# Kernel optimization log

Hardware: AMD Instinct MI355X
Metric: run time of the kernel (lower is better)

The kernel has to match this reference:

```python
import jax, jax.numpy as jnp
import numpy as np

N_NODES = 50000
N_EDGES = 600000
D_IN = 128
D_HID = 128
D_OUT = 64


def setup_inputs() -> dict:
    key = jax.random.key(0)
    ks = jax.random.split(key, 8)
    x = jax.random.normal(ks[0], (N_NODES, D_IN), dtype=jnp.float32)
    edge_index = jax.random.randint(ks[1], (2, N_EDGES), 0, N_NODES, dtype=jnp.int32)
    s = 0.05
    W1l = jax.random.normal(ks[2], (D_HID, D_IN), dtype=jnp.float32) * s
    b1 = jnp.zeros((D_HID,), dtype=jnp.float32)
    W1r = jax.random.normal(ks[3], (D_HID, D_IN), dtype=jnp.float32) * s
    W2l = jax.random.normal(ks[4], (D_OUT, D_HID), dtype=jnp.float32) * s
    b2 = jnp.zeros((D_OUT,), dtype=jnp.float32)
    W2r = jax.random.normal(ks[5], (D_OUT, D_HID), dtype=jnp.float32) * s
    return {"x": x, "edge_index": edge_index, "W1l": W1l, "b1": b1,
            "W1r": W1r, "W2l": W2l, "b2": b2, "W2r": W2r}


def _sage_conv(x, src, dst, Wl, bl, Wr, n_nodes):
    # mean aggregation of source features at destination nodes
    msg_sum = jax.ops.segment_sum(x[src], dst, num_segments=n_nodes)  # [N, D]
    deg = jax.ops.segment_sum(jnp.ones((src.shape[0], 1), x.dtype), dst,
                              num_segments=n_nodes)                   # [N, 1]
    mean = msg_sum / jnp.maximum(deg, 1.0)
    # out = lin_l(mean_neighbors) + lin_r(x_self); bias only on lin_l (PyG default)
    return mean @ Wl.T + bl + x @ Wr.T


def reference(x, edge_index, W1l, b1, W1r, W2l, b2, W2r):
    src, dst = edge_index[0], edge_index[1]
    n = x.shape[0]
    h = jax.nn.relu(_sage_conv(x, src, dst, W1l, b1, W1r, n))
    # dropout p=0.5 is identity in eval mode (training=False)
    return _sage_conv(h, src, dst, W2l, b2, W2r, n)
```

## Files before the change

kernel.cpp:

```cpp
#include <hip/hip_runtime.h>
#include <hip/hip_bf16.h>

typedef __bf16 bf16x8 __attribute__((ext_vector_type(8)));
typedef float f32x4 __attribute__((ext_vector_type(4)));

#define D_FEAT 128
#define MT_STRIDE 136
#define CHUNK 1024

__device__ __forceinline__ float bf16_to_f(unsigned int u16) {
    union { unsigned int i; float f; } c; c.i = u16 << 16; return c.f;
}
__device__ __forceinline__ unsigned short f_to_bf16(float f) {
    __hip_bfloat16 h = (__hip_bfloat16)f;
    return *(unsigned short*)&h;
}
__device__ __forceinline__ float ld(const void* p, int is16, size_t i) {
    return is16 ? (float)((const __hip_bfloat16*)p)[i] : ((const float*)p)[i];
}

__global__ void probe_kernel(const void* x, int* flags) {
    if (threadIdx.x < 64) {
        const unsigned short* u = (const unsigned short*)x;
        unsigned short v = u[threadIdx.x * 2];
        int e = (v >> 7) & 0xFF;
        bool plaus = (e >= 100 && e <= 140);
        unsigned long long m = __ballot(plaus);
        if (threadIdx.x == 0) {
            flags[0] = (__popcll(m) >= 48) ? 1 : 0;
            flags[1] = 1;
        }
    }
}

__global__ void prep_kernel(const void* W1l, const void* b1, const void* W1r,
                            const void* W2l, const void* b2, const void* W2r,
                            const int* __restrict__ flags, unsigned short* wout) {
    int i = blockIdx.x * blockDim.x + threadIdx.x;
    if (i >= 49344) return;
    const int is16 = flags[0];
    const void* s; int base;
    if      (i < 16384) { s = W1l; base = 0; }
    else if (i < 32768) { s = W1r; base = 16384; }
    else if (i < 40960) { s = W2l; base = 32768; }
    else if (i < 49152) { s = W2r; base = 40960; }
    else if (i < 49280) { s = b1;  base = 49152; }
    else                { s = b2;  base = 49280; }
    wout[i] = f_to_bf16(ld(s, is16, i - base));
}

__global__ void conv_kernel(const void* x, const int* __restrict__ flags,
                            unsigned short* __restrict__ xb, int n4) {
    int i = blockIdx.x * blockDim.x + threadIdx.x;
    if (i >= n4) return;
    if (flags[0]) {
        ((uint2*)xb)[i] = ((const uint2*)x)[i];
    } else {
        const float4 v = ((const float4*)x)[i];
        union { unsigned short us[4]; uint2 u; } t;
        t.us[0] = f_to_bf16(v.x); t.us[1] = f_to_bf16(v.y);
        t.us[2] = f_to_bf16(v.z); t.us[3] = f_to_bf16(v.w);
        ((uint2*)xb)[i] = t.u;
    }
}

__global__ void count_deg_kernel(const int* __restrict__ dst, int* __restrict__ deg, int E) {
    int i = blockIdx.x * blockDim.x + threadIdx.x;
    if (i < E) atomicAdd(&deg[dst[i]], 1);
}

__global__ void scan1_kernel(const int* __restrict__ deg, int* __restrict__ bsum, int n) {
    __shared__ int ws[4];
    const int lane = threadIdx.x & 63, wv = threadIdx.x >> 6;
    int i0 = blockIdx.x * CHUNK + threadIdx.x * 4;
    int s = 0;
    #pragma unroll
    for (int j = 0; j < 4; ++j) if (i0 + j < n) s += deg[i0 + j];
    #pragma unroll
    for (int d = 1; d < 64; d <<= 1) s += __shfl_xor(s, d, 64);
    if (lane == 0) ws[wv] = s;
    __syncthreads();
    if (threadIdx.x == 0) bsum[blockIdx.x] = ws[0] + ws[1] + ws[2] + ws[3];
}

__global__ void scan2_kernel(int* __restrict__ bsum, int nb) {
    int lane = threadIdx.x;
    int v = (lane < nb) ? bsum[lane] : 0;
    int sc = v;
    #pragma unroll
    for (int s = 1; s < 64; s <<= 1) {
        int t = __shfl_up(sc, s, 64);
        if (lane >= s) sc += t;
    }
    if (lane < nb) bsum[lane] = sc - v;
}

__global__ void scan3_kernel(const int* __restrict__ deg, const int* __restrict__ bsum,
                             int* __restrict__ off, int* __restrict__ cursor, int n, int E) {
    __shared__ int ws[4];
    const int lane = threadIdx.x & 63, wv = threadIdx.x >> 6;
    int i0 = blockIdx.x * CHUNK + threadIdx.x * 4;
    int v0 = (i0 + 0 < n) ? deg[i0 + 0] : 0;
    int v1 = (i0 + 1 < n) ? deg[i0 + 1] : 0;
    int v2 = (i0 + 2 < n) ? deg[i0 + 2] : 0;
    int v3 = (i0 + 3 < n) ? deg[i0 + 3] : 0;
    int tsum = v0 + v1 + v2 + v3;
    int sc = tsum;
    #pragma unroll
    for (int s = 1; s < 64; s <<= 1) {
        int t = __shfl_up(sc, s, 64);
        if (lane >= s) sc += t;
    }
    if (lane == 63) ws[wv] = sc;
    __syncthreads();
    int woff = 0;
    for (int w = 0; w < wv; ++w) woff += ws[w];
    int p = bsum[blockIdx.x] + woff + (sc - tsum);
    if (i0 + 0 < n) { off[i0 + 0] = p; cursor[i0 + 0] = p; p += v0; }
    if (i0 + 1 < n) { off[i0 + 1] = p; cursor[i0 + 1] = p; p += v1; }
    if (i0 + 2 < n) { off[i0 + 2] = p; cursor[i0 + 2] = p; p += v2; }
    if (i0 + 3 < n) { off[i0 + 3] = p; cursor[i0 + 3] = p; p += v3; }
    if (blockIdx.x == 0 && threadIdx.x == 0) off[n] = E;
}

__global__ void fill_kernel(const int* __restrict__ src, const int* __restrict__ dst,
                            int* __restrict__ cursor, int* __restrict__ esrc, int E) {
    int i = blockIdx.x * blockDim.x + threadIdx.x;
    if (i < E) {
        int p = atomicAdd(&cursor[dst[i]], 1);
        esrc[p] = src[i];
    }
}

template <int NOUT, bool RELU>
__global__ __launch_bounds__(512)
void fused_layer_kernel(const void* feat, const int* __restrict__ flagp,
                        const int* __restrict__ off, const int* __restrict__ esrc,
                        const unsigned short* __restrict__ Wl,
                        const unsigned short* __restrict__ Wr,
                        const unsigned short* __restrict__ bias,
                        const int* __restrict__ oflag,
                        void* __restrict__ out, int N) {
    __shared__ unsigned short meanT[64][MT_STRIDE];
    const int tid = threadIdx.x;
    const int lane = tid & 63;
    const int wave = tid >> 6;
    const int is16 = flagp[0];
    const int o16 = oflag[0];
    const int node0 = blockIdx.x * 64;

    const int a_lo = node0 + wave * 8;
    if (a_lo < N) {
        const int a_hi = min(a_lo + 8, N);
        int offv = off[min(a_lo + min(lane, 8), N)];
        #define OFFAT(i) __shfl(offv, (i), 64)
        const int e_end = OFFAT(a_hi - a_lo);
        int e = OFFAT(0);
        int g = a_lo;
        int gstart = e;
        int gend = OFFAT(1);
        float ax = 0.f, ay = 0.f;
        for (; e < e_end; e += 8) {
            int sk[8];
            #pragma unroll
            for (int k = 0; k < 8; ++k) sk[k] = esrc[min(e + k, e_end - 1)];
            float rx[8], ry[8];
            if (is16) {
                #pragma unroll
                for (int k = 0; k < 8; ++k) {
                    unsigned int u = ((const unsigned int*)
                        ((const unsigned short*)feat + (size_t)sk[k] * D_FEAT))[lane];
                    rx[k] = bf16_to_f(u & 0xffffu);
                    ry[k] = bf16_to_f(u >> 16);
                }
            } else {
                #pragma unroll
                for (int k = 0; k < 8; ++k) {
                    float2 v = ((const float2*)
                        ((const float*)feat + (size_t)sk[k] * D_FEAT))[lane];
                    rx[k] = v.x; ry[k] = v.y;
                }
            }
            #pragma unroll
            for (int k = 0; k < 8; ++k) {
                if (e + k < e_end) {
                    while (e + k >= gend) {
                        int d = gend - gstart;
                        float inv = 1.f / (float)(d > 0 ? d : 1);
                        unsigned int pk = (unsigned int)f_to_bf16(ax * inv)
                                        | ((unsigned int)f_to_bf16(ay * inv) << 16);
                        *(unsigned int*)&meanT[g - node0][lane * 2] = pk;
                        ax = ay = 0.f;
                        ++g; gstart = gend;
                        gend = OFFAT(min(g - a_lo + 1, 8));
                    }
                    ax += rx[k]; ay += ry[k];
                }
            }
        }
        while (g < a_hi) {
            int d = gend - gstart;
            float inv = 1.f / (float)(d > 0 ? d : 1);
            unsigned int pk = (unsigned int)f_to_bf16(ax * inv)
                            | ((unsigned int)f_to_bf16(ay * inv) << 16);
            *(unsigned int*)&meanT[g - node0][lane * 2] = pk;
            ax = ay = 0.f;
            ++g; gstart = gend;
            gend = OFFAT(min(g - a_lo + 1, 8));
        }
        #undef OFFAT
    }
    __syncthreads();

    const int rowg = wave >> 1;
    const int colh = wave & 1;
    constexpr int NT = NOUT / 32;
    const int n_lo = node0 + rowg * 16;
    const int lrow = lane & 15;
    const int kg = lane >> 4;
    f32x4 acc[NT];
    #pragma unroll
    for (int t = 0; t < NT; ++t) acc[t] = (f32x4){0.f, 0.f, 0.f, 0.f};

    const int grow = min(n_lo + lrow, N - 1);
    #pragma unroll
    for (int hh = 0; hh < 2; ++hh) {
        const unsigned short* W = hh ? Wr : Wl;
        #pragma unroll
        for (int ks = 0; ks < 4; ++ks) {
            const int k0 = ks * 32 + kg * 8;
            bf16x8 a;
            if (hh == 0) {
                a = *(const bf16x8*)&meanT[rowg * 16 + lrow][k0];
            } else if (is16) {
                a = *(const bf16x8*)((const unsigned short*)feat + (size_t)grow * D_FEAT + k0);
            } else {
                const float* fp = (const float*)feat + (size_t)grow * D_FEAT + k0;
                union { bf16x8 v; unsigned short us[8]; } t;
                #pragma unroll
                for (int j = 0; j < 8; ++j) t.us[j] = f_to_bf16(fp[j]);
                a = t.v;
            }
            #pragma unroll
            for (int t = 0; t < NT; ++t) {
                int col16 = colh * NT + t;
                bf16x8 b = *(const bf16x8*)(W + (size_t)(col16 * 16 + lrow) * D_FEAT + k0);
                acc[t] = __builtin_amdgcn_mfma_f32_16x16x32_bf16(a, b, acc[t], 0, 0, 0);
            }
        }
    }
    const int orow0 = n_lo + kg * 4;
    #pragma unroll
    for (int t = 0; t < NT; ++t) {
        const int col = (colh * NT + t) * 16 + lrow;
        float bv = bf16_to_f(bias[col]);
        #pragma unroll
        for (int r = 0; r < 4; ++r) {
            int orow = orow0 + r;
            if (orow < N) {
                float v = acc[t][r] + bv;
                if (RELU) v = fmaxf(v, 0.f);
                if (o16) ((__hip_bfloat16*)out)[(size_t)orow * NOUT + col] = (__hip_bfloat16)v;
                else     ((float*)out)[(size_t)orow * NOUT + col] = v;
            }
        }
    }
}

extern "C" void kernel_launch(void* const* d_in, const int* in_sizes, int n_in,
                              void* d_out, int out_size, void* d_ws, size_t ws_size,
                              hipStream_t stream) {
    const void* x   = d_in[0];
    const int* eidx = (const int*)d_in[1];
    const void* W1l = d_in[2];
    const void* b1  = d_in[3];
    const void* W1r = d_in[4];
    const void* W2l = d_in[5];
    const void* b2  = d_in[6];
    const void* W2r = d_in[7];

    const int N = in_sizes[0] / D_FEAT;
    const int E = in_sizes[1] / 2;
    const int* src = eidx;
    const int* dst = eidx + E;

    char* ws = (char*)d_ws;
    size_t o = 0;
    auto alloc = [&](size_t bytes) -> void* {
        void* p = ws + o;
        o += (bytes + 255) & ~(size_t)255;
        return p;
    };
    int* flags  = (int*)alloc(256);
    int* bsum   = (int*)alloc(64 * 4);
    int* deg    = (int*)alloc((size_t)N * 4);
    int* off    = (int*)alloc((size_t)(N + 1) * 4);
    int* cursor = (int*)alloc((size_t)N * 4);
    int* esrc   = (int*)alloc((size_t)E * 4);
    unsigned short* wconv = (unsigned short*)alloc(49344 * 2);
    __hip_bfloat16* h = (__hip_bfloat16*)alloc((size_t)N * D_FEAT * 2);
    unsigned short* xb = (unsigned short*)alloc((size_t)N * D_FEAT * 2);
    const bool use_xb = (o <= ws_size);
    (void)n_in; (void)out_size;

    probe_kernel<<<1, 64, 0, stream>>>(x, flags);
    prep_kernel<<<(49344 + 255) / 256, 256, 0, stream>>>(W1l, b1, W1r, W2l, b2, W2r, flags, wconv);
    hipMemsetAsync(deg, 0, (size_t)N * 4, stream);
    count_deg_kernel<<<(E + 255) / 256, 256, 0, stream>>>(dst, deg, E);
    const int nchunk = (N + CHUNK - 1) / CHUNK;
    scan1_kernel<<<nchunk, 256, 0, stream>>>(deg, bsum, N);
    scan2_kernel<<<1, 64, 0, stream>>>(bsum, nchunk);
    scan3_kernel<<<nchunk, 256, 0, stream>>>(deg, bsum, off, cursor, N, E);
    fill_kernel<<<(E + 255) / 256, 256, 0, stream>>>(src, dst, cursor, esrc, E);

    const void* feat1;
    const int* flag1;
    if (use_xb) {
        const int n4 = N * D_FEAT / 4;
        conv_kernel<<<(n4 + 255) / 256, 256, 0, stream>>>(x, flags, xb, n4);
        feat1 = xb; flag1 = flags + 1;
    } else {
        feat1 = x; flag1 = flags + 0;
    }

    const int nblocks = (N + 63) / 64;
    fused_layer_kernel<128, true><<<nblocks, 512, 0, stream>>>(
        feat1, flag1, off, esrc,
        wconv + 0, wconv + 16384, wconv + 49152, flags + 1, h, N);
    fused_layer_kernel<64, false><<<nblocks, 512, 0, stream>>>(
        h, flags + 1, off, esrc,
        wconv + 32768, wconv + 40960, wconv + 49280, flags + 0, d_out, N);
}
```

Measured before the change: 274.5 us.

## Pad CSR segments to multiples of four and gather with 16-byte loads

Each node's edge list is padded to a multiple of four entries. The padding entries point to a new all-zero dummy row N, so one wave can gather four neighbour rows at once, with each 16-lane quarter loading a uint4 per row. Partial sums are reduced across the quarters with shuffles, and the mean divides by the true degree. Blocks shrink to 32 nodes and 256 threads, and the fp32 feature path is dropped in favour of always using the bf16 copy. This adds a fillpad pass, a zero-row kernel and extra padded edge traffic.

```diff
diff --git a/kernel.cpp b/kernel.cpp
--- a/kernel.cpp
+++ b/kernel.cpp
@@ -8,8 +8,8 @@
 #define MT_STRIDE 136
 #define CHUNK 1024
 
-__device__ __forceinline__ float bf16_to_f(unsigned int u16) {
-    union { unsigned int i; float f; } c; c.i = u16 << 16; return c.f;
+__device__ __forceinline__ float bits_to_f(unsigned int u) {
+    union { unsigned int i; float f; } c; c.i = u; return c.f;
 }
 __device__ __forceinline__ unsigned short f_to_bf16(float f) {
     __hip_bfloat16 h = (__hip_bfloat16)f;
@@ -64,6 +64,12 @@
     }
 }
 
+__global__ void zero_rows_kernel(unsigned short* xb, unsigned short* h, int N) {
+    int t = threadIdx.x;
+    xb[(size_t)N * D_FEAT + t] = 0;
+    h[(size_t)N * D_FEAT + t] = 0;
+}
+
 __global__ void count_deg_kernel(const int* __restrict__ dst, int* __restrict__ deg, int E) {
     int i = blockIdx.x * blockDim.x + threadIdx.x;
     if (i < E) atomicAdd(&deg[dst[i]], 1);
@@ -75,7 +81,8 @@
     int i0 = blockIdx.x * CHUNK + threadIdx.x * 4;
     int s = 0;
     #pragma unroll
-    for (int j = 0; j < 4; ++j) if (i0 + j < n) s += deg[i0 + j];
+    for (int j = 0; j < 4; ++j)
+        if (i0 + j < n) { int d = deg[i0 + j]; s += (d + 3) & ~3; }
     #pragma unroll
     for (int d = 1; d < 64; d <<= 1) s += __shfl_xor(s, d, 64);
     if (lane == 0) ws[wv] = s;
@@ -83,7 +90,7 @@
     if (threadIdx.x == 0) bsum[blockIdx.x] = ws[0] + ws[1] + ws[2] + ws[3];
 }
 
-__global__ void scan2_kernel(int* __restrict__ bsum, int nb) {
+__global__ void scan2_kernel(int* __restrict__ bsum, int nb, int* __restrict__ off, int n) {
     int lane = threadIdx.x;
     int v = (lane < nb) ? bsum[lane] : 0;
     int sc = v;
@@ -92,18 +99,20 @@
         int t = __shfl_up(sc, s, 64);
         if (lane >= s) sc += t;
     }
+    if (lane == nb - 1) off[n] = sc;
     if (lane < nb) bsum[lane] = sc - v;
 }
 
 __global__ void scan3_kernel(const int* __restrict__ deg, const int* __restrict__ bsum,
-                             int* __restrict__ off, int* __restrict__ cursor, int n, int E) {
+                             int* __restrict__ off, int* __restrict__ cursor, int n) {
     __shared__ int ws[4];
     const int lane = threadIdx.x & 63, wv = threadIdx.x >> 6;
     int i0 = blockIdx.x * CHUNK + threadIdx.x * 4;
-    int v0 = (i0 + 0 < n) ? deg[i0 + 0] : 0;
-    int v1 = (i0 + 1 < n) ? deg[i0 + 1] : 0;
-    int v2 = (i0 + 2 < n) ? deg[i0 + 2] : 0;
-    int v3 = (i0 + 3 < n) ? deg[i0 + 3] : 0;
+    int v0 = 0, v1 = 0, v2 = 0, v3 = 0;
+    if (i0 + 0 < n) v0 = (deg[i0 + 0] + 3) & ~3;
+    if (i0 + 1 < n) v1 = (deg[i0 + 1] + 3) & ~3;
+    if (i0 + 2 < n) v2 = (deg[i0 + 2] + 3) & ~3;
+    if (i0 + 3 < n) v3 = (deg[i0 + 3] + 3) & ~3;
     int tsum = v0 + v1 + v2 + v3;
     int sc = tsum;
     #pragma unroll
@@ -120,7 +129,6 @@
     if (i0 + 1 < n) { off[i0 + 1] = p; cursor[i0 + 1] = p; p += v1; }
     if (i0 + 2 < n) { off[i0 + 2] = p; cursor[i0 + 2] = p; p += v2; }
     if (i0 + 3 < n) { off[i0 + 3] = p; cursor[i0 + 3] = p; p += v3; }
-    if (blockIdx.x == 0 && threadIdx.x == 0) off[n] = E;
 }
 
 __global__ void fill_kernel(const int* __restrict__ src, const int* __restrict__ dst,
@@ -132,80 +140,96 @@
     }
 }
 
+__global__ void fillpad_kernel(const int* __restrict__ off, const int* __restrict__ deg,
+                               int* __restrict__ esrc, int N) {
+    int g = blockIdx.x * blockDim.x + threadIdx.x;
+    if (g >= N) return;
+    int s = off[g] + deg[g];
+    int e = off[g] + ((deg[g] + 3) & ~3);
+    for (int i = s; i < e; ++i) esrc[i] = N;
+}
+
 template <int NOUT, bool RELU>
-__global__ __launch_bounds__(512)
-void fused_layer_kernel(const void* feat, const int* __restrict__ flagp,
-                        const int* __restrict__ off, const int* __restrict__ esrc,
+__global__ __launch_bounds__(256)
+void fused_layer_kernel(const unsigned short* __restrict__ feat,
+                        const int* __restrict__ off, const int* __restrict__ deg,
+                        const int* __restrict__ esrc,
                         const unsigned short* __restrict__ Wl,
                         const unsigned short* __restrict__ Wr,
                         const unsigned short* __restrict__ bias,
                         const int* __restrict__ oflag,
                         void* __restrict__ out, int N) {
-    __shared__ unsigned short meanT[64][MT_STRIDE];
+    __shared__ unsigned short meanT[32][MT_STRIDE];
     const int tid = threadIdx.x;
     const int lane = tid & 63;
     const int wave = tid >> 6;
-    const int is16 = flagp[0];
+    const int node0 = blockIdx.x * 32;
     const int o16 = oflag[0];
-    const int node0 = blockIdx.x * 64;
 
     const int a_lo = node0 + wave * 8;
     if (a_lo < N) {
         const int a_hi = min(a_lo + 8, N);
+        const int nn = a_hi - a_lo;
         int offv = off[min(a_lo + min(lane, 8), N)];
+        int degv = deg[min(a_lo + min(lane, 7), N - 1)];
         #define OFFAT(i) __shfl(offv, (i), 64)
-        const int e_end = OFFAT(a_hi - a_lo);
-        int e = OFFAT(0);
+        const int e_beg = OFFAT(0);
+        const int e_end = OFFAT(nn);
+        const int quarter = lane >> 4;
+        const int fl = lane & 15;
+        float ax[8];
+        #pragma unroll
+        for (int i = 0; i < 8; ++i) ax[i] = 0.f;
         int g = a_lo;
-        int gstart = e;
         int gend = OFFAT(1);
-        float ax = 0.f, ay = 0.f;
-        for (; e < e_end; e += 8) {
-            int sk[8];
+
+        auto flush = [&](int gg) {
+            int td = __shfl(degv, gg - a_lo, 64);
+            float inv = 1.f / (float)(td > 0 ? td : 1);
+            unsigned int pk[4];
             #pragma unroll
-            for (int k = 0; k < 8; ++k) sk[k] = esrc[min(e + k, e_end - 1)];
-            float rx[8], ry[8];
-            if (is16) {
-                #pragma unroll
-                for (int k = 0; k < 8; ++k) {
-                    unsigned int u = ((const unsigned int*)
-                        ((const unsigned short*)feat + (size_t)sk[k] * D_FEAT))[lane];
-                    rx[k] = bf16_to_f(u & 0xffffu);
-                    ry[k] = bf16_to_f(u >> 16);
-                }
-            } else {
-                #pragma unroll
-                for (int k = 0; k < 8; ++k) {
-                    float2 v = ((const float2*)
-                        ((const float*)feat + (size_t)sk[k] * D_FEAT))[lane];
-                    rx[k] = v.x; ry[k] = v.y;
-                }
-            }
+            for (int i = 0; i < 4; ++i) {
+                float v0 = ax[2 * i], v1 = ax[2 * i + 1];
+                v0 += __shfl_xor(v0, 16, 64); v0 += __shfl_xor(v0, 32, 64);
+                v1 += __shfl_xor(v1, 16, 64); v1 += __shfl_xor(v1, 32, 64);
+                pk[i] = (unsigned int)f_to_bf16(v0 * inv)
+                      | ((unsigned int)f_to_bf16(v1 * inv) << 16);
+                ax[2 * i] = 0.f; ax[2 * i + 1] = 0.f;
+            }
+            if (quarter == 0)
+                *(uint4*)&meanT[gg - node0][fl * 8] = make_uint4(pk[0], pk[1], pk[2], pk[3]);
+        };
+
+        int cur = (e_beg < e_end) ? esrc[min(e_beg + (lane & 31), e_end - 1)] : 0;
+        for (int e = e_beg; e < e_end; e += 32) {
+            int nxt = (e + 32 < e_end) ? esrc[min(e + 32 + (lane & 31), e_end - 1)] : 0;
+            uint4 r[8];
             #pragma unroll
             for (int k = 0; k < 8; ++k) {
-                if (e + k < e_end) {
-                    while (e + k >= gend) {
-                        int d = gend - gstart;
-                        float inv = 1.f / (float)(d > 0 ? d : 1);
-                        unsigned int pk = (unsigned int)f_to_bf16(ax * inv)
-                                        | ((unsigned int)f_to_bf16(ay * inv) << 16);
-                        *(unsigned int*)&meanT[g - node0][lane * 2] = pk;
-                        ax = ay = 0.f;
-                        ++g; gstart = gend;
+                int sk = __shfl(cur, 4 * k + quarter, 64);
+                r[k] = *(const uint4*)(feat + (size_t)sk * D_FEAT + fl * 8);
+            }
+            #pragma unroll
+            for (int k = 0; k < 8; ++k) {
+                const int eb = e + 4 * k;
+                if (eb < e_end) {
+                    while (eb >= gend) {
+                        flush(g);
+                        ++g;
                         gend = OFFAT(min(g - a_lo + 1, 8));
                     }
-                    ax += rx[k]; ay += ry[k];
+                    uint4 u = r[k];
+                    ax[0] += bits_to_f(u.x << 16); ax[1] += bits_to_f(u.x & 0xffff0000u);
+                    ax[2] += bits_to_f(u.y << 16); ax[3] += bits_to_f(u.y & 0xffff0000u);
+                    ax[4] += bits_to_f(u.z << 16); ax[5] += bits_to_f(u.z & 0xffff0000u);
+                    ax[6] += bits_to_f(u.w << 16); ax[7] += bits_to_f(u.w & 0xffff0000u);
                 }
             }
+            cur = nxt;
         }
         while (g < a_hi) {
-            int d = gend - gstart;
-            float inv = 1.f / (float)(d > 0 ? d : 1);
-            unsigned int pk = (unsigned int)f_to_bf16(ax * inv)
-                            | ((unsigned int)f_to_bf16(ay * inv) << 16);
-            *(unsigned int*)&meanT[g - node0][lane * 2] = pk;
-            ax = ay = 0.f;
-            ++g; gstart = gend;
+            flush(g);
+            ++g;
             gend = OFFAT(min(g - a_lo + 1, 8));
         }
         #undef OFFAT
@@ -222,7 +246,7 @@
     #pragma unroll
     for (int t = 0; t < NT; ++t) acc[t] = (f32x4){0.f, 0.f, 0.f, 0.f};
 
-    const int grow = min(n_lo + lrow, N - 1);
+    const int grow = min(n_lo + lrow, N);
     #pragma unroll
     for (int hh = 0; hh < 2; ++hh) {
         const unsigned short* W = hh ? Wr : Wl;
@@ -230,17 +254,8 @@
         for (int ks = 0; ks < 4; ++ks) {
             const int k0 = ks * 32 + kg * 8;
             bf16x8 a;
-            if (hh == 0) {
-                a = *(const bf16x8*)&meanT[rowg * 16 + lrow][k0];
-            } else if (is16) {
-                a = *(const bf16x8*)((const unsigned short*)feat + (size_t)grow * D_FEAT + k0);
-            } else {
-                const float* fp = (const float*)feat + (size_t)grow * D_FEAT + k0;
-                union { bf16x8 v; unsigned short us[8]; } t;
-                #pragma unroll
-                for (int j = 0; j < 8; ++j) t.us[j] = f_to_bf16(fp[j]);
-                a = t.v;
-            }
+            if (hh == 0) a = *(const bf16x8*)&meanT[rowg * 16 + lrow][k0];
+            else         a = *(const bf16x8*)(feat + (size_t)grow * D_FEAT + k0);
             #pragma unroll
             for (int t = 0; t < NT; ++t) {
                 int col16 = colh * NT + t;
@@ -253,12 +268,12 @@
     #pragma unroll
     for (int t = 0; t < NT; ++t) {
         const int col = (colh * NT + t) * 16 + lrow;
-        float bv = bf16_to_f(bias[col]);
+        float bv = bits_to_f((unsigned int)bias[col] << 16);
         #pragma unroll
-        for (int r = 0; r < 4; ++r) {
-            int orow = orow0 + r;
+        for (int r2 = 0; r2 < 4; ++r2) {
+            int orow = orow0 + r2;
             if (orow < N) {
-                float v = acc[t][r] + bv;
+                float v = acc[t][r2] + bv;
                 if (RELU) v = fmaxf(v, 0.f);
                 if (o16) ((__hip_bfloat16*)out)[(size_t)orow * NOUT + col] = (__hip_bfloat16)v;
                 else     ((float*)out)[(size_t)orow * NOUT + col] = v;
@@ -296,12 +311,11 @@
     int* deg    = (int*)alloc((size_t)N * 4);
     int* off    = (int*)alloc((size_t)(N + 1) * 4);
     int* cursor = (int*)alloc((size_t)N * 4);
-    int* esrc   = (int*)alloc((size_t)E * 4);
+    int* esrc   = (int*)alloc((size_t)(E + 3 * N + 64) * 4);
     unsigned short* wconv = (unsigned short*)alloc(49344 * 2);
-    __hip_bfloat16* h = (__hip_bfloat16*)alloc((size_t)N * D_FEAT * 2);
-    unsigned short* xb = (unsigned short*)alloc((size_t)N * D_FEAT * 2);
-    const bool use_xb = (o <= ws_size);
-    (void)n_in; (void)out_size;
+    unsigned short* h  = (unsigned short*)alloc((size_t)(N + 1) * D_FEAT * 2);
+    unsigned short* xb = (unsigned short*)alloc((size_t)(N + 1) * D_FEAT * 2);
+    (void)n_in; (void)out_size; (void)ws_size;
 
     probe_kernel<<<1, 64, 0, stream>>>(x, flags);
     prep_kernel<<<(49344 + 255) / 256, 256, 0, stream>>>(W1l, b1, W1r, W2l, b2, W2r, flags, wconv);
@@ -309,25 +323,20 @@
     count_deg_kernel<<<(E + 255) / 256, 256, 0, stream>>>(dst, deg, E);
     const int nchunk = (N + CHUNK - 1) / CHUNK;
     scan1_kernel<<<nchunk, 256, 0, stream>>>(deg, bsum, N);
-    scan2_kernel<<<1, 64, 0, stream>>>(bsum, nchunk);
-    scan3_kernel<<<nchunk, 256, 0, stream>>>(deg, bsum, off, cursor, N, E);
+    scan2_kernel<<<1, 64, 0, stream>>>(bsum, nchunk, off, N);
+    scan3_kernel<<<nchunk, 256, 0, stream>>>(deg, bsum, off, cursor, N);
     fill_kernel<<<(E + 255) / 256, 256, 0, stream>>>(src, dst, cursor, esrc, E);
-
-    const void* feat1;
-    const int* flag1;
-    if (use_xb) {
-        const int n4 = N * D_FEAT / 4;
-        conv_kernel<<<(n4 + 255) / 256, 256, 0, stream>>>(x, flags, xb, n4);
-        feat1 = xb; flag1 = flags + 1;
-    } else {
-        feat1 = x; flag1 = flags + 0;
-    }
-
-    const int nblocks = (N + 63) / 64;
-    fused_layer_kernel<128, true><<<nblocks, 512, 0, stream>>>(
-        feat1, flag1, off, esrc,
+    fillpad_kernel<<<(N + 255) / 256, 256, 0, stream>>>(off, deg, esrc, N);
+
+    const int n4 = N * D_FEAT / 4;
+    conv_kernel<<<(n4 + 255) / 256, 256, 0, stream>>>(x, flags, xb, n4);
+    zero_rows_kernel<<<1, 128, 0, stream>>>(xb, h, N);
+
+    const int nblocks = (N + 31) / 32;
+    fused_layer_kernel<128, true><<<nblocks, 256, 0, stream>>>(
+        xb, off, deg, esrc,
         wconv + 0, wconv + 16384, wconv + 49152, flags + 1, h, N);
-    fused_layer_kernel<64, false><<<nblocks, 512, 0, stream>>>(
-        h, flags + 1, off, esrc,
+    fused_layer_kernel<64, false><<<nblocks, 256, 0, stream>>>(
+        h, off, deg, esrc,
         wconv + 32768, wconv + 40960, wconv + 49280, flags + 0, d_out, N);
 }
```

After: 249.6 us. 9.1% less time.
